# Kernel tuning notes

Hardware: AMD Instinct MI355X
Metric: run time of the kernel (lower is better)

## Reference

```python
import jax, jax.numpy as jnp
import numpy as np

N_NODES = 100000
N_EDGES = 1600000
D = 128
L = 3


def setup_inputs() -> dict:
    key = jax.random.key(0)
    k1, k2, k3 = jax.random.split(key, 3)
    edge_index = jax.random.randint(k1, (2, N_EDGES), 0, N_NODES, dtype=jnp.int64)
    emb = jax.random.normal(k2, (N_NODES, D), dtype=jnp.float32)
    # Glorot-style scale for the per-layer linear weights
    Ws = jax.random.normal(k3, (L, D, D), dtype=jnp.float32) * (1.0 / np.sqrt(D))
    bs = jnp.zeros((L, D), dtype=jnp.float32)
    return {"edge_index": edge_index, "emb": emb, "Ws": Ws, "bs": bs}


def _gcn_forward(emb, Ws, bs, edge_index):
    n = emb.shape[0]
    self_loop = jnp.arange(n, dtype=edge_index.dtype)
    # PyG GCNConv adds self-loops and uses symmetric normalization
    row = jnp.concatenate([edge_index[0], self_loop])  # source nodes
    col = jnp.concatenate([edge_index[1], self_loop])  # target nodes
    deg = jax.ops.segment_sum(jnp.ones(row.shape[0], dtype=emb.dtype), col, num_segments=n)
    deg_inv_sqrt = jnp.where(deg > 0, jax.lax.rsqrt(jnp.maximum(deg, 1.0)), 0.0)
    norm = deg_inv_sqrt[row] * deg_inv_sqrt[col]  # [E+N]

    x = emb
    for l in range(Ws.shape[0]):
        h = x @ Ws[l]                              # [N, D] linear transform
        msg = h[row] * norm[:, None]               # gather + scale [E+N, D]
        x = jax.ops.segment_sum(msg, col, num_segments=n) + bs[l]  # scatter-add
        x = jax.nn.relu(x)                         # dropout is identity in eval
    return x


def reference(edge_index, emb, Ws, bs) -> jnp.ndarray:
    return _gcn_forward(emb, Ws, bs, edge_index)
```

## Files before the change

### kernel.cpp

```cpp
#include <hip/hip_runtime.h>
#include <hip/hip_fp16.h>
#include <cstdint>
#include <cstddef>

#define N_NODES 100000
#define N_EDGES 1600000
#define D 128
#define NLAYERS 3
#define NB 3125
#define NBLK_E 128
#define EPB 12500
#define ENT_CAP 1024

typedef float f2v __attribute__((ext_vector_type(2)));
typedef float f4v __attribute__((ext_vector_type(4)));
typedef _Float16 f16x8 __attribute__((ext_vector_type(8)));
typedef float f32x4 __attribute__((ext_vector_type(4)));


__global__ __launch_bounds__(512) void hist1_kernel(const int* __restrict__ col,
                                                    int* __restrict__ hmat) {
    __shared__ int hist[NB];
    int b = blockIdx.x, t = threadIdx.x;
    for (int j = t; j < NB; j += 512) hist[j] = 0;
    __syncthreads();
    int base = b * EPB;
    for (int i = t; i < EPB; i += 512) {
        int c = col[base + i];
        atomicAdd(&hist[c >> 5], 1);
    }
    __syncthreads();
    for (int j = t; j < NB; j += 512) hmat[b * NB + j] = hist[j];
}

__global__ void btot_kernel(const int* __restrict__ hmat, int* __restrict__ btot) {
    int j = blockIdx.x * 256 + threadIdx.x;
    if (j < NB) {
        int s = 0;
        for (int b = 0; b < NBLK_E; b++) s += hmat[b * NB + j];
        btot[j] = s;
    }
}

__global__ void bscan_kernel(const int* __restrict__ btot, int* __restrict__ bstart, int nb, int e) {
    __shared__ int lsum[1024];
    int t = threadIdx.x;
    int vals[4];
    int v0 = 0;
#pragma unroll
    for (int j = 0; j < 4; j++) {
        int idx = t * 4 + j;
        int c = (idx < nb) ? btot[idx] : 0;
        vals[j] = c;
        v0 += c;
    }
    lsum[t] = v0;
    __syncthreads();
    for (int off = 1; off < 1024; off <<= 1) {
        int x = (t >= off) ? lsum[t - off] : 0;
        __syncthreads();
        lsum[t] += x;
        __syncthreads();
    }
    int base = lsum[t] - v0;
#pragma unroll
    for (int j = 0; j < 4; j++) {
        int idx = t * 4 + j;
        if (idx < nb) {
            bstart[idx] = base;
            base += vals[j];
        }
    }
    if (t == 0) bstart[nb] = e;
}

__global__ void hoff_kernel(const int* __restrict__ hmat, const int* __restrict__ bstart,
                            int* __restrict__ hoff) {
    int j = blockIdx.x * 256 + threadIdx.x;
    if (j < NB) {
        int run = bstart[j];
        for (int b = 0; b < NBLK_E; b++) {
            hoff[b * NB + j] = run;
            run += hmat[b * NB + j];
        }
    }
}

__global__ __launch_bounds__(512) void scatter_kernel(const int* __restrict__ row,
                                                      const int* __restrict__ col,
                                                      const int* __restrict__ hoff,
                                                      unsigned* __restrict__ bucketbuf) {
    __shared__ int cur[NB];
    int b = blockIdx.x, t = threadIdx.x;
    for (int j = t; j < NB; j += 512) cur[j] = hoff[b * NB + j];
    __syncthreads();
    int base = b * EPB;
    for (int i = t; i < EPB; i += 512) {
        int r = row[base + i], c = col[base + i];
        int pos = atomicAdd(&cur[c >> 5], 1);
        bucketbuf[pos] = ((unsigned)r << 5) | (unsigned)(c & 31);
    }
}

__global__ void fill2_kernel(const unsigned* __restrict__ bucketbuf, const int* __restrict__ bstart,
                             int* __restrict__ offsets, float* __restrict__ dinv,
                             int* __restrict__ src, int n, int e) {
    __shared__ unsigned ent[ENT_CAP];
    __shared__ int hist[32];
    __shared__ int cur[32];
    __shared__ int loff[32];
    int b = blockIdx.x, t = threadIdx.x;
    int s0 = bstart[b];
    int cnt = bstart[b + 1] - s0;
    if (cnt > ENT_CAP) cnt = ENT_CAP;
    if (t < 32) hist[t] = 0;
    __syncthreads();
    for (int i = t; i < cnt; i += 256) {
        unsigned v = bucketbuf[s0 + i];
        ent[i] = v;
        atomicAdd(&hist[v & 31], 1);
    }
    __syncthreads();
    if (t == 0) {
        int run = s0;
#pragma unroll
        for (int j = 0; j < 32; j++) {
            loff[j] = run;
            run += hist[j];
        }
    }
    __syncthreads();
    if (t < 32) {
        int node = b * 32 + t;
        int o = loff[t];
        offsets[node] = o;
        cur[t] = o;
        dinv[node] = rsqrtf((float)(hist[t] + 1));
    }
    if (b == 0 && t == 0) offsets[n] = e;
    __syncthreads();
    for (int i = t; i < cnt; i += 256) {
        unsigned v = ent[i];
        int pos = atomicAdd(&cur[v & 31], 1);
        src[pos] = (int)(v >> 5);
    }
}


__global__ void cast_kernel(const float2* __restrict__ in, const float* __restrict__ dinv,
                            __half2* __restrict__ out, int n2) {
    int i = blockIdx.x * 256 + threadIdx.x;
    if (i < n2) {
        float d = dinv[i >> 6];
        float2 v = in[i];
        out[i] = __floats2half2_rn(d * v.x, d * v.y);
    }
}

__global__ void wsplit_kernel(const float* __restrict__ W,
                              _Float16* __restrict__ Wh, _Float16* __restrict__ Wl) {
    int c = blockIdx.x, l = blockIdx.y, k = threadIdx.x;
    float w = W[(size_t)l * 16384 + k * 128 + c];
    _Float16 h = (_Float16)w;
    float r = w - (float)h;
    Wh[(size_t)l * 16384 + c * 128 + k] = h;
    Wl[(size_t)l * 16384 + c * 128 + k] = (_Float16)r;
}

__global__ __launch_bounds__(256, 8) void agg_gemm_kernel(
    const __half2* __restrict__ xs_in, const int* __restrict__ offs,
    const int* __restrict__ src, const float* __restrict__ dinv,
    const _Float16* __restrict__ Whp, const _Float16* __restrict__ Wlp,
    const float* __restrict__ bias, float* __restrict__ out,
    __half2* __restrict__ xs_out, int write_h, int write_out) {
    __shared__ _Float16 sA[2][16][136];
    int t = threadIdx.x;
    int f = t & 63;
    int w = t >> 6;
    int r0 = blockIdx.x * 16;

#pragma unroll 1
    for (int q = 0; q < 4; q++) {
        int lr = w * 4 + q;
        int v = r0 + lr;
        float dv = dinv[v];
        float2 a0 = __half22float2(xs_in[(size_t)v * 64 + f]);
        float ax = a0.x;
        float ay = a0.y;
        int i = offs[v], s1 = offs[v + 1];
        for (; i + 7 < s1; i += 8) {
            int s[8];
#pragma unroll
            for (int j = 0; j < 8; j++) s[j] = src[i + j];
            float2 x[8];
#pragma unroll
            for (int j = 0; j < 8; j++) x[j] = __half22float2(xs_in[(size_t)s[j] * 64 + f]);
#pragma unroll
            for (int j = 0; j < 8; j++) {
                ax += x[j].x;
                ay += x[j].y;
            }
        }
        if (i < s1) {
            int last = s1 - 1;
            int s[8];
            float m[8];
#pragma unroll
            for (int j = 0; j < 8; j++) {
                int idx = i + j;
                bool in = idx < s1;
                s[j] = src[in ? idx : last];
                m[j] = in ? 1.0f : 0.0f;
            }
            float2 x[8];
#pragma unroll
            for (int j = 0; j < 8; j++) x[j] = __half22float2(xs_in[(size_t)s[j] * 64 + f]);
#pragma unroll
            for (int j = 0; j < 8; j++) {
                ax += m[j] * x[j].x;
                ay += m[j] * x[j].y;
            }
        }
        float rx = dv * ax, ry = dv * ay;
        __half2 h2 = __floats2half2_rn(rx, ry);
        float2 hb = __half22float2(h2);
        __half2 l2 = __floats2half2_rn(rx - hb.x, ry - hb.y);
        *(unsigned*)&sA[0][lr][2 * f] = __builtin_bit_cast(unsigned, h2);
        *(unsigned*)&sA[1][lr][2 * f] = __builtin_bit_cast(unsigned, l2);
    }
    __syncthreads();

    int lrow = f & 15, kg = f >> 4;
    f32x4 acc[2];
    acc[0] = (f32x4){0.f, 0.f, 0.f, 0.f};
    acc[1] = (f32x4){0.f, 0.f, 0.f, 0.f};

#pragma unroll
    for (int ks = 0; ks < 4; ks++) {
        int g = ks * 4 + kg;
        f16x8 ah = *(const f16x8*)&sA[0][lrow][g * 8];
        f16x8 al = *(const f16x8*)&sA[1][lrow][g * 8];
#pragma unroll
        for (int c = 0; c < 2; c++) {
            int col = (w * 2 + c) * 16 + lrow;
            f16x8 bh = *(const f16x8*)&Whp[(size_t)col * 128 + g * 8];
            f16x8 bl = *(const f16x8*)&Wlp[(size_t)col * 128 + g * 8];
            acc[c] = __builtin_amdgcn_mfma_f32_16x16x32_f16(ah, bh, acc[c], 0, 0, 0);
            acc[c] = __builtin_amdgcn_mfma_f32_16x16x32_f16(al, bh, acc[c], 0, 0, 0);
            acc[c] = __builtin_amdgcn_mfma_f32_16x16x32_f16(ah, bl, acc[c], 0, 0, 0);
        }
    }

    float bcol[2];
    bcol[0] = bias[(w * 2 + 0) * 16 + lrow];
    bcol[1] = bias[(w * 2 + 1) * 16 + lrow];
    int rbase = r0 + kg * 4;
#pragma unroll
    for (int j = 0; j < 4; j++) {
        int rowi = rbase + j;
        float dvr = write_h ? dinv[rowi] : 0.f;
#pragma unroll
        for (int c = 0; c < 2; c++) {
            float o = fmaxf(acc[c][j] + bcol[c], 0.f);
            float o2 = __shfl_xor(o, 1);
            int col = (w * 2 + c) * 16 + lrow;
            if (write_out)
                __builtin_nontemporal_store(o, out + (size_t)rowi * 128 + col);
            if (write_h && !(f & 1))
                xs_out[(size_t)rowi * 64 + (col >> 1)] =
                    __floats2half2_rn(dvr * o, dvr * o2);
        }
    }
}


extern "C" void kernel_launch(void* const* d_in, const int* in_sizes, int n_in,
                              void* d_out, int out_size, void* d_ws, size_t ws_size,
                              hipStream_t stream) {
    const int* edge = (const int*)d_in[0];
    const float* emb = (const float*)d_in[1];
    const float* Ws = (const float*)d_in[2];
    const float* bs = (const float*)d_in[3];
    float* out = (float*)d_out;

    const int n = N_NODES, e = N_EDGES;
    const int* row = edge;
    const int* col = edge + e;

    char* p = (char*)d_ws;
    __half2* xsA = (__half2*)p;
    unsigned* bucketbuf = (unsigned*)p;
    p += (size_t)n * D * 2;
    __half2* xsB = (__half2*)p;
    p += (size_t)n * D * 2;
    int* csr_src  = (int*)p;    p += (size_t)e * 4;
    float* dinv   = (float*)p;  p += (size_t)n * 4;
    int* offsets  = (int*)p;    p += (size_t)(n + 1) * 4;
    int* btot     = (int*)p;    p += (size_t)NB * 4;
    int* bstart   = (int*)p;    p += (size_t)(NB + 1) * 4;
    int* hmat     = (int*)p;    p += (size_t)NBLK_E * NB * 4;
    int* hoff     = (int*)p;    p += (size_t)NBLK_E * NB * 4;
    _Float16* WhT = (_Float16*)p; p += (size_t)NLAYERS * D * D * 2;
    _Float16* WlT = (_Float16*)p; p += (size_t)NLAYERS * D * D * 2;

    hist1_kernel<<<NBLK_E, 512, 0, stream>>>(col, hmat);
    btot_kernel<<<(NB + 255) / 256, 256, 0, stream>>>(hmat, btot);
    bscan_kernel<<<1, 1024, 0, stream>>>(btot, bstart, NB, e);
    hoff_kernel<<<(NB + 255) / 256, 256, 0, stream>>>(hmat, bstart, hoff);
    scatter_kernel<<<NBLK_E, 512, 0, stream>>>(row, col, hoff, bucketbuf);
    fill2_kernel<<<NB, 256, 0, stream>>>(bucketbuf, bstart, offsets, dinv, csr_src, n, e);
    wsplit_kernel<<<dim3(128, NLAYERS), 128, 0, stream>>>(Ws, WhT, WlT);

    int n2 = n * 64;
    cast_kernel<<<(n2 + 255) / 256, 256, 0, stream>>>((const float2*)emb, dinv, xsA, n2);

    __half2* xin = xsA;
    __half2* xout = xsB;
    for (int l = 0; l < NLAYERS; l++) {
        agg_gemm_kernel<<<n / 16, 256, 0, stream>>>(
            xin, offsets, csr_src, dinv,
            WhT + (size_t)l * D * D, WlT + (size_t)l * D * D,
            bs + (size_t)l * D, out, xout,
            (l < NLAYERS - 1) ? 1 : 0, (l == NLAYERS - 1) ? 1 : 0);
        __half2* tmp = xin; xin = xout; xout = tmp;
    }
}
```

Measured before the change: 496.3 us.

## Split fused aggregation+GEMM into separate per-node gather and 32-row MFMA GEMM kernels

```diff
diff --git a/kernel.cpp b/kernel.cpp
--- a/kernel.cpp
+++ b/kernel.cpp
@@ -16,6 +16,7 @@
 typedef float f4v __attribute__((ext_vector_type(4)));
 typedef _Float16 f16x8 __attribute__((ext_vector_type(8)));
 typedef float f32x4 __attribute__((ext_vector_type(4)));
+typedef unsigned u32x4 __attribute__((ext_vector_type(4)));
 
 
 __global__ __launch_bounds__(512) void hist1_kernel(const int* __restrict__ col,
@@ -167,108 +168,131 @@
     Wl[(size_t)l * 16384 + c * 128 + k] = (_Float16)r;
 }
 
-__global__ __launch_bounds__(256, 8) void agg_gemm_kernel(
-    const __half2* __restrict__ xs_in, const int* __restrict__ offs,
-    const int* __restrict__ src, const float* __restrict__ dinv,
+__global__ void agg_kernel(const __half2* __restrict__ xs, const int* __restrict__ offs,
+                           unsigned* __restrict__ Ah, unsigned* __restrict__ Al,
+                           const float* __restrict__ dinv, const int* __restrict__ src) {
+    int v = blockIdx.x;
+    int f = threadIdx.x;
+    float dv = dinv[v];
+    float2 a0 = __half22float2(xs[(size_t)v * 64 + f]);
+    float ax = a0.x;
+    float ay = a0.y;
+    int i = offs[v], s1 = offs[v + 1];
+    for (; i + 7 < s1; i += 8) {
+        int s[8];
+#pragma unroll
+        for (int j = 0; j < 8; j++) s[j] = src[i + j];
+        float2 x[8];
+#pragma unroll
+        for (int j = 0; j < 8; j++) x[j] = __half22float2(xs[(size_t)s[j] * 64 + f]);
+#pragma unroll
+        for (int j = 0; j < 8; j++) {
+            ax += x[j].x;
+            ay += x[j].y;
+        }
+    }
+    if (i < s1) {
+        int last = s1 - 1;
+        int s[8];
+        float m[8];
+#pragma unroll
+        for (int j = 0; j < 8; j++) {
+            int idx = i + j;
+            bool in = idx < s1;
+            s[j] = src[in ? idx : last];
+            m[j] = in ? 1.0f : 0.0f;
+        }
+        float2 x[8];
+#pragma unroll
+        for (int j = 0; j < 8; j++) x[j] = __half22float2(xs[(size_t)s[j] * 64 + f]);
+#pragma unroll
+        for (int j = 0; j < 8; j++) {
+            ax += m[j] * x[j].x;
+            ay += m[j] * x[j].y;
+        }
+    }
+    float rx = dv * ax, ry = dv * ay;
+    __half2 h2 = __floats2half2_rn(rx, ry);
+    float2 hb = __half22float2(h2);
+    __half2 l2 = __floats2half2_rn(rx - hb.x, ry - hb.y);
+    __builtin_nontemporal_store(__builtin_bit_cast(unsigned, h2), Ah + (size_t)v * 64 + f);
+    __builtin_nontemporal_store(__builtin_bit_cast(unsigned, l2), Al + (size_t)v * 64 + f);
+}
+
+__global__ __launch_bounds__(256, 6) void gemm_mfma_kernel(
+    const _Float16* __restrict__ Ahp, const _Float16* __restrict__ Alp,
     const _Float16* __restrict__ Whp, const _Float16* __restrict__ Wlp,
     const float* __restrict__ bias, float* __restrict__ out,
-    __half2* __restrict__ xs_out, int write_h, int write_out) {
-    __shared__ _Float16 sA[2][16][136];
+    __half2* __restrict__ xs_out, const float* __restrict__ dinv,
+    int write_h, int write_out) {
+    __shared__ _Float16 sA[2][32][136];
     int t = threadIdx.x;
     int f = t & 63;
     int w = t >> 6;
-    int r0 = blockIdx.x * 16;
-
-#pragma unroll 1
-    for (int q = 0; q < 4; q++) {
-        int lr = w * 4 + q;
-        int v = r0 + lr;
-        float dv = dinv[v];
-        float2 a0 = __half22float2(xs_in[(size_t)v * 64 + f]);
-        float ax = a0.x;
-        float ay = a0.y;
-        int i = offs[v], s1 = offs[v + 1];
-        for (; i + 7 < s1; i += 8) {
-            int s[8];
-#pragma unroll
-            for (int j = 0; j < 8; j++) s[j] = src[i + j];
-            float2 x[8];
-#pragma unroll
-            for (int j = 0; j < 8; j++) x[j] = __half22float2(xs_in[(size_t)s[j] * 64 + f]);
-#pragma unroll
-            for (int j = 0; j < 8; j++) {
-                ax += x[j].x;
-                ay += x[j].y;
-            }
-        }
-        if (i < s1) {
-            int last = s1 - 1;
-            int s[8];
-            float m[8];
-#pragma unroll
-            for (int j = 0; j < 8; j++) {
-                int idx = i + j;
-                bool in = idx < s1;
-                s[j] = src[in ? idx : last];
-                m[j] = in ? 1.0f : 0.0f;
-            }
-            float2 x[8];
-#pragma unroll
-            for (int j = 0; j < 8; j++) x[j] = __half22float2(xs_in[(size_t)s[j] * 64 + f]);
-#pragma unroll
-            for (int j = 0; j < 8; j++) {
-                ax += m[j] * x[j].x;
-                ay += m[j] * x[j].y;
-            }
-        }
-        float rx = dv * ax, ry = dv * ay;
-        __half2 h2 = __floats2half2_rn(rx, ry);
-        float2 hb = __half22float2(h2);
-        __half2 l2 = __floats2half2_rn(rx - hb.x, ry - hb.y);
-        *(unsigned*)&sA[0][lr][2 * f] = __builtin_bit_cast(unsigned, h2);
-        *(unsigned*)&sA[1][lr][2 * f] = __builtin_bit_cast(unsigned, l2);
+    int row0 = blockIdx.x * 32;
+
+    const u32x4* Aq[2] = {(const u32x4*)Ahp, (const u32x4*)Alp};
+#pragma unroll
+    for (int i = 0; i < 4; i++) {
+        int qid = t + 256 * i;
+        int p = qid >> 9;
+        int rem = qid & 511;
+        int r = rem >> 4;
+        int k2 = rem & 15;
+        u32x4 v = __builtin_nontemporal_load(&Aq[p][(size_t)(row0 + r) * 16 + k2]);
+        *(u32x4*)&sA[p][r][k2 * 8] = v;
     }
     __syncthreads();
 
     int lrow = f & 15, kg = f >> 4;
-    f32x4 acc[2];
-    acc[0] = (f32x4){0.f, 0.f, 0.f, 0.f};
-    acc[1] = (f32x4){0.f, 0.f, 0.f, 0.f};
+    f32x4 acc[2][2];
+#pragma unroll
+    for (int m = 0; m < 2; m++)
+#pragma unroll
+        for (int c = 0; c < 2; c++) acc[m][c] = (f32x4){0.f, 0.f, 0.f, 0.f};
 
 #pragma unroll
     for (int ks = 0; ks < 4; ks++) {
         int g = ks * 4 + kg;
-        f16x8 ah = *(const f16x8*)&sA[0][lrow][g * 8];
-        f16x8 al = *(const f16x8*)&sA[1][lrow][g * 8];
+        f16x8 a0h = *(const f16x8*)&sA[0][lrow][g * 8];
+        f16x8 a0l = *(const f16x8*)&sA[1][lrow][g * 8];
+        f16x8 a1h = *(const f16x8*)&sA[0][16 + lrow][g * 8];
+        f16x8 a1l = *(const f16x8*)&sA[1][16 + lrow][g * 8];
 #pragma unroll
         for (int c = 0; c < 2; c++) {
-            int col = (w * 2 + c) * 16 + lrow;
+            int col = w * 32 + c * 16 + lrow;
             f16x8 bh = *(const f16x8*)&Whp[(size_t)col * 128 + g * 8];
             f16x8 bl = *(const f16x8*)&Wlp[(size_t)col * 128 + g * 8];
-            acc[c] = __builtin_amdgcn_mfma_f32_16x16x32_f16(ah, bh, acc[c], 0, 0, 0);
-            acc[c] = __builtin_amdgcn_mfma_f32_16x16x32_f16(al, bh, acc[c], 0, 0, 0);
-            acc[c] = __builtin_amdgcn_mfma_f32_16x16x32_f16(ah, bl, acc[c], 0, 0, 0);
+            acc[0][c] = __builtin_amdgcn_mfma_f32_16x16x32_f16(a0h, bh, acc[0][c], 0, 0, 0);
+            acc[0][c] = __builtin_amdgcn_mfma_f32_16x16x32_f16(a0l, bh, acc[0][c], 0, 0, 0);
+            acc[0][c] = __builtin_amdgcn_mfma_f32_16x16x32_f16(a0h, bl, acc[0][c], 0, 0, 0);
+            acc[1][c] = __builtin_amdgcn_mfma_f32_16x16x32_f16(a1h, bh, acc[1][c], 0, 0, 0);
+            acc[1][c] = __builtin_amdgcn_mfma_f32_16x16x32_f16(a1l, bh, acc[1][c], 0, 0, 0);
+            acc[1][c] = __builtin_amdgcn_mfma_f32_16x16x32_f16(a1h, bl, acc[1][c], 0, 0, 0);
         }
     }
 
     float bcol[2];
-    bcol[0] = bias[(w * 2 + 0) * 16 + lrow];
-    bcol[1] = bias[(w * 2 + 1) * 16 + lrow];
-    int rbase = r0 + kg * 4;
-#pragma unroll
-    for (int j = 0; j < 4; j++) {
-        int rowi = rbase + j;
-        float dvr = write_h ? dinv[rowi] : 0.f;
-#pragma unroll
-        for (int c = 0; c < 2; c++) {
-            float o = fmaxf(acc[c][j] + bcol[c], 0.f);
-            float o2 = __shfl_xor(o, 1);
-            int col = (w * 2 + c) * 16 + lrow;
-            if (write_out)
-                __builtin_nontemporal_store(o, out + (size_t)rowi * 128 + col);
-            if (write_h && !(f & 1))
-                xs_out[(size_t)rowi * 64 + (col >> 1)] =
-                    __floats2half2_rn(dvr * o, dvr * o2);
+    bcol[0] = bias[w * 32 + 0 * 16 + lrow];
+    bcol[1] = bias[w * 32 + 1 * 16 + lrow];
+#pragma unroll
+    for (int m = 0; m < 2; m++) {
+        int rbase = row0 + m * 16 + kg * 4;
+#pragma unroll
+        for (int j = 0; j < 4; j++) {
+            int rowi = rbase + j;
+            float dvr = write_h ? dinv[rowi] : 0.f;
+#pragma unroll
+            for (int c = 0; c < 2; c++) {
+                float o = fmaxf(acc[m][c][j] + bcol[c], 0.f);
+                float o2 = __shfl_xor(o, 1);
+                int col = w * 32 + c * 16 + lrow;
+                if (write_out)
+                    __builtin_nontemporal_store(o, out + (size_t)rowi * 128 + col);
+                if (write_h && !(f & 1))
+                    xs_out[(size_t)rowi * 64 + (col >> 1)] =
+                        __floats2half2_rn(dvr * o, dvr * o2);
+            }
         }
     }
 }
@@ -288,18 +312,20 @@
     const int* col = edge + e;
 
     char* p = (char*)d_ws;
-    __half2* xsA = (__half2*)p;
+    _Float16* Ah = (_Float16*)p;
+    int* hmat = (int*)p;
+    int* hoff = hmat + (size_t)NBLK_E * NB;
+    p += (size_t)n * D * 2;
+    _Float16* Al = (_Float16*)p;
+    p += (size_t)n * D * 2;
+    __half2* xs = (__half2*)p;
     unsigned* bucketbuf = (unsigned*)p;
-    p += (size_t)n * D * 2;
-    __half2* xsB = (__half2*)p;
     p += (size_t)n * D * 2;
     int* csr_src  = (int*)p;    p += (size_t)e * 4;
     float* dinv   = (float*)p;  p += (size_t)n * 4;
     int* offsets  = (int*)p;    p += (size_t)(n + 1) * 4;
     int* btot     = (int*)p;    p += (size_t)NB * 4;
     int* bstart   = (int*)p;    p += (size_t)(NB + 1) * 4;
-    int* hmat     = (int*)p;    p += (size_t)NBLK_E * NB * 4;
-    int* hoff     = (int*)p;    p += (size_t)NBLK_E * NB * 4;
     _Float16* WhT = (_Float16*)p; p += (size_t)NLAYERS * D * D * 2;
     _Float16* WlT = (_Float16*)p; p += (size_t)NLAYERS * D * D * 2;
 
@@ -312,16 +338,14 @@
     wsplit_kernel<<<dim3(128, NLAYERS), 128, 0, stream>>>(Ws, WhT, WlT);
 
     int n2 = n * 64;
-    cast_kernel<<<(n2 + 255) / 256, 256, 0, stream>>>((const float2*)emb, dinv, xsA, n2);
-
-    __half2* xin = xsA;
-    __half2* xout = xsB;
+    cast_kernel<<<(n2 + 255) / 256, 256, 0, stream>>>((const float2*)emb, dinv, xs, n2);
+
     for (int l = 0; l < NLAYERS; l++) {
-        agg_gemm_kernel<<<n / 16, 256, 0, stream>>>(
-            xin, offsets, csr_src, dinv,
-            WhT + (size_t)l * D * D, WlT + (size_t)l * D * D,
-            bs + (size_t)l * D, out, xout,
+        agg_kernel<<<n, 64, 0, stream>>>(xs, offsets, (unsigned*)Ah, (unsigned*)Al,
+                                         dinv, csr_src);
+        gemm_mfma_kernel<<<n / 32, 256, 0, stream>>>(
+            Ah, Al, WhT + (size_t)l * D * D, WlT + (size_t)l * D * D,
+            bs + (size_t)l * D, out, xs, dinv,
             (l < NLAYERS - 1) ? 1 : 0, (l == NLAYERS - 1) ? 1 : 0);
-        __half2* tmp = xin; xin = xout; xout = tmp;
-    }
-}
+    }
+}
```

Measured after the change: 499.5 us. About the same (+0.7%).
